# Optimization experiments

Measured on AMD Instinct MI355X. Metric: run time of the kernel, lower is better.

The kernel has to match this reference:

```python
import jax, jax.numpy as jnp
import numpy as np

B, C, H, W = 32, 512, 28, 28
NC, NM, K = 50, 4, 5          # num_classes, num_mixtures, num_clutter_models
OCC = 0.3                     # occ_likely[0]


def setup_inputs() -> dict:
    key = jax.random.key(0)
    k1, k2, k3 = jax.random.split(key, 3)
    x = jax.random.uniform(k1, (B, C, H, W), dtype=jnp.float32)
    mix_model = jax.random.uniform(k2, (NC * NM, C, H, W), dtype=jnp.float32)
    clutter_model = jax.random.uniform(k3, (K, C), dtype=jnp.float32)
    return {"x": x, "mix_model": mix_model, "clutter_model": clutter_model}


def _l1_normalize(a, axis):
    # torch: F.normalize(torch.clamp(a, 0, 1), p=1, dim=axis) with eps=1e-12
    a = jnp.clip(a, 0.0, 1.0)
    return a / jnp.maximum(jnp.sum(a, axis=axis, keepdims=True), 1e-12)


def reference(x, mix_model, clutter_model):
    # clutter: [K, C] -> L1-normalized over channels
    cl = _l1_normalize(clutter_model, axis=1)
    # background log-likelihood: (x.unsqueeze(1) * cl[:, :, None, None]).sum(2)
    bg = jnp.einsum('bchw,kc->bkhw', x, cl)            # [B, K, H, W]
    bg = jnp.log(bg * OCC + 1e-10)
    # mixture models: [M, C, H, W] -> L1-normalized over channels
    mm = _l1_normalize(mix_model, axis=1)
    # foreground log-likelihood: (x.unsqueeze(1) * mm).sum(2)
    fg = jnp.einsum('bchw,mchw->bmhw', x, mm)          # [B, M, H, W]
    fg = jnp.log(fg * (1.0 - OCC) + 1e-10)
    fg = fg.reshape(B, NC, NM, 1, H, W)
    # per-pixel occlusion max between foreground and background, sum over H, W
    per_model = jnp.maximum(fg, bg[:, None, None, :, :, :]).sum((-1, -2))  # [B, NC, NM, K]
    # max over clutter models, then over mixtures
    return per_model.max(axis=-1).max(axis=-1)          # [B, NC]
```

## Files before the change

kernel.cpp:

```cpp
#include <hip/hip_runtime.h>
#include <math.h>

#define Bc  32
#define Cc  512
#define HWc 784
#define Mc  200
#define Kc  5
#define NCc 50

#define PTm   16
#define MTm   16
#define NMB   13
#define NPB   49
#define CKm   32
#define NCHm  16
#define RSTR  18
#define XPL   (32*RSTR)
#define MPL   (16*RSTR)
#define MMBASE (16*XPL)
#define LDSDW (16*XPL + 16*MPL)

typedef short s8v __attribute__((ext_vector_type(8)));
typedef float f4v __attribute__((ext_vector_type(4)));

union F8 { uint2 u2[2]; s8v h; };

__device__ __forceinline__ unsigned f2b(float f) {
    union { float f; unsigned u; } v; v.f = f;
    return (v.u + 0x7FFFu + ((v.u >> 16) & 1u)) >> 16;
}
__device__ __forceinline__ unsigned pk(float lo, float hi) {
    return f2b(lo) | (f2b(hi) << 16);
}

__global__ __launch_bounds__(256) void k_bg(const float* __restrict__ x,
                                            const float* __restrict__ clut,
                                            float* __restrict__ bgpart) {
    __shared__ float cl[Kc * Cc];
    __shared__ float csum[Kc];
    const int t = threadIdx.x;
    for (int i = t; i < Kc * Cc; i += 256) cl[i] = clut[i];
    __syncthreads();
    if (t < 160) {
        const int k = t >> 5, l = t & 31;
        float s = 0.0f;
        for (int c = l; c < Cc; c += 32) s += cl[k * Cc + c];
#pragma unroll
        for (int off = 16; off > 0; off >>= 1) s += __shfl_down(s, off, 32);
        if (l == 0) csum[k] = fmaxf(s, 1e-12f);
    }
    __syncthreads();

    const int b = blockIdx.x;
    const int z = blockIdx.z;
    const int hw = blockIdx.y * 256 + t;
    if (hw < HWc) {
        float acc[Kc] = {0.f, 0.f, 0.f, 0.f, 0.f};
        const int cbase = z * 128;
        const float* xb = x + ((size_t)b * Cc + cbase) * HWc + hw;
#pragma unroll 4
        for (int c = 0; c < 128; ++c) {
            const float xv = xb[c * HWc];
#pragma unroll
            for (int k = 0; k < Kc; ++k) acc[k] = fmaf(xv, cl[k * Cc + cbase + c], acc[k]);
        }
#pragma unroll
        for (int k = 0; k < Kc; ++k)
            bgpart[(((z * Bc + b) * Kc) + k) * HWc + hw] = acc[k] / csum[k];
    }
}

__global__ void k_bgsum(const float* __restrict__ bgpart, float* __restrict__ bgl) {
    const int i = blockIdx.x * 256 + threadIdx.x;
    const int N = Bc * Kc * HWc;
    if (i < N) {
        const float s = bgpart[i] + bgpart[i + N] + bgpart[i + 2 * N] + bgpart[i + 3 * N];
        bgl[i] = logf(0.3f * s + 1e-10f);
    }
}

__global__ __launch_bounds__(256) __attribute__((amdgpu_waves_per_eu(2, 2)))
void k_fg(const float* __restrict__ x, const float* __restrict__ mm,
          float* __restrict__ fg) {
    __shared__ unsigned lds[LDSDW];

    const int t = threadIdx.x;

    const int nwg = NMB * NPB;
    const int q = nwg >> 3, r = nwg & 7;
    const int xcd = blockIdx.x & 7, sidx = blockIdx.x >> 3;
    const int wgid = (xcd < r ? xcd * (q + 1) : r * (q + 1) + (xcd - r) * q) + sidx;
    const int mblk = wgid % NMB;
    const int pix0 = (wgid / NMB) * PTm;

    int xoff[4], xl[4];
#pragma unroll
    for (int g = 0; g < 4; ++g) {
        const int G = t + 256 * g;
        const int qq = G & 3, b = (G >> 2) & 31, cg = G >> 7;
        xoff[g] = (b * Cc + cg * 4) * HWc + pix0 + 4 * qq;
        xl[g]   = 4 * qq * XPL + b * RSTR + cg * 2;
    }
    int moff[2], ml[2];
    float mzero[2];
#pragma unroll
    for (int g = 0; g < 2; ++g) {
        const int G = t + 256 * g;
        const int qq = G & 3, mr = (G >> 2) & 15, cg = (G >> 6) & 7;
        const int mrow = mblk * MTm + mr;
        mzero[g] = (mrow < Mc) ? 1.0f : 0.0f;
        const int mc = (mrow < Mc) ? mrow : (Mc - 1);
        moff[g] = (mc * Cc + cg * 4) * HWc + pix0 + 4 * qq;
        ml[g]   = MMBASE + 4 * qq * MPL + mr * RSTR + cg * 2;
    }

    const int lane = t & 63;
    const int w    = t >> 6;
    const int row18q = (lane & 15) * RSTR + (lane >> 4) * 4;

    f4v accD[4][2], accS[4];
#pragma unroll
    for (int p = 0; p < 4; ++p) {
        accS[p] = (f4v)0.0f;
#pragma unroll
        for (int bt = 0; bt < 2; ++bt) accD[p][bt] = (f4v)0.0f;
    }
    const s8v ones = {0x3F80, 0x3F80, 0x3F80, 0x3F80, 0x3F80, 0x3F80, 0x3F80, 0x3F80};

    float4 LX[4][4], LM[2][4];
#pragma unroll
    for (int g = 0; g < 4; ++g)
#pragma unroll
        for (int cc = 0; cc < 4; ++cc)
            LX[g][cc] = *(const float4*)(x + xoff[g] + cc * HWc);
#pragma unroll
    for (int g = 0; g < 2; ++g)
#pragma unroll
        for (int cc = 0; cc < 4; ++cc)
            LM[g][cc] = *(const float4*)(mm + moff[g] + cc * HWc);
#pragma unroll
    for (int g = 0; g < 4; ++g) xoff[g] += CKm * HWc;
#pragma unroll
    for (int g = 0; g < 2; ++g) moff[g] += CKm * HWc;

#pragma unroll 1
    for (int ch = 0; ch < NCHm; ++ch) {
        __syncthreads();

#pragma unroll
        for (int g = 0; g < 4; ++g) {
            const float* f0 = (const float*)&LX[g][0];
            const float* f1 = (const float*)&LX[g][1];
            const float* f2 = (const float*)&LX[g][2];
            const float* f3 = (const float*)&LX[g][3];
#pragma unroll
            for (int p = 0; p < 4; ++p)
                *(uint2*)&lds[xl[g] + p * XPL] =
                    make_uint2(pk(f0[p], f1[p]), pk(f2[p], f3[p]));
        }
#pragma unroll
        for (int g = 0; g < 2; ++g) {
            const float z = mzero[g];
            const float* f0 = (const float*)&LM[g][0];
            const float* f1 = (const float*)&LM[g][1];
            const float* f2 = (const float*)&LM[g][2];
            const float* f3 = (const float*)&LM[g][3];
#pragma unroll
            for (int p = 0; p < 4; ++p)
                *(uint2*)&lds[ml[g] + p * MPL] =
                    make_uint2(pk(f0[p] * z, f1[p] * z), pk(f2[p] * z, f3[p] * z));
        }

        if (ch + 1 < NCHm) {
#pragma unroll
            for (int g = 0; g < 4; ++g)
#pragma unroll
                for (int cc = 0; cc < 4; ++cc)
                    LX[g][cc] = *(const float4*)(x + xoff[g] + cc * HWc);
#pragma unroll
            for (int g = 0; g < 2; ++g)
#pragma unroll
                for (int cc = 0; cc < 4; ++cc)
                    LM[g][cc] = *(const float4*)(mm + moff[g] + cc * HWc);
#pragma unroll
            for (int g = 0; g < 4; ++g) xoff[g] += CKm * HWc;
#pragma unroll
            for (int g = 0; g < 2; ++g) moff[g] += CKm * HWc;
        }

        __syncthreads();

#pragma unroll
        for (int p = 0; p < 4; ++p) {
            const int pixg = w * 4 + p;
            const unsigned* Xp = &lds[pixg * XPL + row18q];
            const unsigned* Mp = &lds[MMBASE + pixg * MPL + row18q];
            F8 a0, a1, bf;
            a0.u2[0] = *(const uint2*)(Xp);
            a0.u2[1] = *(const uint2*)(Xp + 2);
            a1.u2[0] = *(const uint2*)(Xp + 16 * RSTR);
            a1.u2[1] = *(const uint2*)(Xp + 16 * RSTR + 2);
            bf.u2[0] = *(const uint2*)(Mp);
            bf.u2[1] = *(const uint2*)(Mp + 2);
            accD[p][0] = __builtin_amdgcn_mfma_f32_16x16x32_bf16(a0.h, bf.h, accD[p][0], 0, 0, 0);
            accD[p][1] = __builtin_amdgcn_mfma_f32_16x16x32_bf16(a1.h, bf.h, accD[p][1], 0, 0, 0);
            accS[p]    = __builtin_amdgcn_mfma_f32_16x16x32_bf16(ones, bf.h, accS[p],    0, 0, 0);
        }
    }

    const int m = mblk * MTm + (lane & 15);
    if (m < Mc) {
        const int quad = lane >> 4;
#pragma unroll
        for (int p = 0; p < 4; ++p) {
            const int hw = pix0 + w * 4 + p;
            const float scale = 0.7f / fmaxf(accS[p][0], 1e-12f);
#pragma unroll
            for (int bt = 0; bt < 2; ++bt)
#pragma unroll
                for (int r = 0; r < 4; ++r) {
                    const int b = bt * 16 + quad * 4 + r;
                    fg[((size_t)m * Bc + b) * HWc + hw] =
                        logf(accD[p][bt][r] * scale + 1e-10f);
                }
        }
    }
}

__global__ __launch_bounds__(256) void k_red(const float* __restrict__ fg,
                                             const float* __restrict__ bgl,
                                             float* __restrict__ pm) {
    const int bm = blockIdx.x;
    const int b = bm / Mc;
    const int m = bm % Mc;
    const int t = threadIdx.x;
    const float* fgp = fg + ((size_t)m * Bc + b) * HWc;
    const float* bgb = bgl + (size_t)b * Kc * HWc;

    float s[Kc] = {0.f, 0.f, 0.f, 0.f, 0.f};
    for (int hw = t; hw < HWc; hw += 256) {
        const float f = fgp[hw];
#pragma unroll
        for (int k = 0; k < Kc; ++k) s[k] += fmaxf(f, bgb[k * HWc + hw]);
    }
#pragma unroll
    for (int off = 32; off > 0; off >>= 1) {
#pragma unroll
        for (int k = 0; k < Kc; ++k) s[k] += __shfl_down(s[k], off, 64);
    }
    __shared__ float red[4][Kc];
    const int wv = t >> 6, ln = t & 63;
    if (ln == 0) {
#pragma unroll
        for (int k = 0; k < Kc; ++k) red[wv][k] = s[k];
    }
    __syncthreads();
    if (t == 0) {
        float best = -INFINITY;
#pragma unroll
        for (int k = 0; k < Kc; ++k)
            best = fmaxf(best, red[0][k] + red[1][k] + red[2][k] + red[3][k]);
        pm[bm] = best;
    }
}

__global__ void k_out(const float* __restrict__ pm, float* __restrict__ out) {
    const int i = blockIdx.x * 256 + threadIdx.x;
    if (i < Bc * NCc) {
        const int b = i / NCc, nc = i % NCc;
        const float* p = pm + (size_t)b * Mc + nc * 4;
        out[i] = fmaxf(fmaxf(p[0], p[1]), fmaxf(p[2], p[3]));
    }
}

extern "C" void kernel_launch(void* const* d_in, const int* in_sizes, int n_in,
                              void* d_out, int out_size, void* d_ws, size_t ws_size,
                              hipStream_t stream) {
    const float* x    = (const float*)d_in[0];
    const float* mixm = (const float*)d_in[1];
    const float* clut = (const float*)d_in[2];
    float* out = (float*)d_out;

    float* fg     = (float*)d_ws;
    float* bgpart = fg + (size_t)Mc * Bc * HWc;
    float* bgl    = bgpart + (size_t)4 * Bc * Kc * HWc;
    float* pm     = bgl + (size_t)Bc * Kc * HWc;

    k_bg   <<<dim3(Bc, 4, 4), 256, 0, stream>>>(x, clut, bgpart);
    k_bgsum<<<dim3((Bc * Kc * HWc + 255) / 256), 256, 0, stream>>>(bgpart, bgl);
    k_fg   <<<dim3(NMB * NPB), 256, 0, stream>>>(x, mixm, fg);
    k_red  <<<dim3(Bc * Mc), 256, 0, stream>>>(fg, bgl, pm);
    k_out  <<<dim3(7), 256, 0, stream>>>(pm, out);
}
```

Measured before the change: 560.6 us.

## Fuse background max-sum reduction into MFMA kernel and swizzle LDS layout

The foreground kernel no longer writes the full [M,B,HW] log-likelihood tensor. It computes the log, takes the max against the background log-likelihoods and sums per pixel in registers, then reduces across waves through LDS into per-pixel-block partials. A small second kernel sums those partials and takes the max over clutter models. This removes a large global write and reread of the foreground tensor. The change also replaces row padding with an XOR swizzle in LDS, staggers the x loads into two halves to lower register pressure, and sets launch bounds to 3 blocks, at the cost of a heavier epilogue and extra scattered reads of the background values.

Result: slower. 636.5 us (+13.6%).

```diff
diff --git a/kernel.cpp b/kernel.cpp
--- a/kernel.cpp
+++ b/kernel.cpp
@@ -14,11 +14,12 @@
 #define NPB   49
 #define CKm   32
 #define NCHm  16
-#define RSTR  18
-#define XPL   (32*RSTR)
-#define MPL   (16*RSTR)
+#define XPL   (32*16)
+#define MPL   (16*16)
 #define MMBASE (16*XPL)
 #define LDSDW (16*XPL + 16*MPL)
+
+#define RSH(row) ((((row) >> 1) & 7) << 1)
 
 typedef short s8v __attribute__((ext_vector_type(8)));
 typedef float f4v __attribute__((ext_vector_type(4)));
@@ -79,9 +80,9 @@
     }
 }
 
-__global__ __launch_bounds__(256) __attribute__((amdgpu_waves_per_eu(2, 2)))
+__global__ __launch_bounds__(256, 3)
 void k_fg(const float* __restrict__ x, const float* __restrict__ mm,
-          float* __restrict__ fg) {
+          const float* __restrict__ bgl, float* __restrict__ pm_part) {
     __shared__ unsigned lds[LDSDW];
 
     const int t = threadIdx.x;
@@ -91,7 +92,8 @@
     const int xcd = blockIdx.x & 7, sidx = blockIdx.x >> 3;
     const int wgid = (xcd < r ? xcd * (q + 1) : r * (q + 1) + (xcd - r) * q) + sidx;
     const int mblk = wgid % NMB;
-    const int pix0 = (wgid / NMB) * PTm;
+    const int pb   = wgid / NMB;
+    const int pix0 = pb * PTm;
 
     int xoff[4], xl[4];
 #pragma unroll
@@ -99,7 +101,7 @@
         const int G = t + 256 * g;
         const int qq = G & 3, b = (G >> 2) & 31, cg = G >> 7;
         xoff[g] = (b * Cc + cg * 4) * HWc + pix0 + 4 * qq;
-        xl[g]   = 4 * qq * XPL + b * RSTR + cg * 2;
+        xl[g]   = 4 * qq * XPL + b * 16 + ((cg * 2) ^ RSH(b));
     }
     int moff[2], ml[2];
     float mzero[2];
@@ -111,12 +113,17 @@
         mzero[g] = (mrow < Mc) ? 1.0f : 0.0f;
         const int mc = (mrow < Mc) ? mrow : (Mc - 1);
         moff[g] = (mc * Cc + cg * 4) * HWc + pix0 + 4 * qq;
-        ml[g]   = MMBASE + 4 * qq * MPL + mr * RSTR + cg * 2;
+        ml[g]   = MMBASE + 4 * qq * MPL + mr * 16 + ((cg * 2) ^ RSH(mr));
     }
 
     const int lane = t & 63;
     const int w    = t >> 6;
-    const int row18q = (lane & 15) * RSTR + (lane >> 4) * 4;
+    const int fr   = lane & 15;
+    const int q4   = (lane >> 4) * 4;
+    const int fsw  = RSH(fr);
+    const int d0   = q4 ^ fsw;
+    const int d1   = (q4 + 2) ^ fsw;
+    const int rowbase = fr * 16;
 
     f4v accD[4][2], accS[4];
 #pragma unroll
@@ -127,37 +134,34 @@
     }
     const s8v ones = {0x3F80, 0x3F80, 0x3F80, 0x3F80, 0x3F80, 0x3F80, 0x3F80, 0x3F80};
 
-    float4 LX[4][4], LM[2][4];
-#pragma unroll
-    for (int g = 0; g < 4; ++g)
+    float4 LXa[2][4], LXb[2][4], LM[2][4];
+#pragma unroll
+    for (int g = 0; g < 2; ++g) {
 #pragma unroll
         for (int cc = 0; cc < 4; ++cc)
-            LX[g][cc] = *(const float4*)(x + xoff[g] + cc * HWc);
-#pragma unroll
-    for (int g = 0; g < 2; ++g)
+            LXa[g][cc] = *(const float4*)(x + xoff[g] + cc * HWc);
+        xoff[g] += CKm * HWc;
+    }
+#pragma unroll
+    for (int g = 0; g < 2; ++g) {
 #pragma unroll
         for (int cc = 0; cc < 4; ++cc)
             LM[g][cc] = *(const float4*)(mm + moff[g] + cc * HWc);
-#pragma unroll
-    for (int g = 0; g < 4; ++g) xoff[g] += CKm * HWc;
-#pragma unroll
-    for (int g = 0; g < 2; ++g) moff[g] += CKm * HWc;
+        moff[g] += CKm * HWc;
+    }
 
 #pragma unroll 1
     for (int ch = 0; ch < NCHm; ++ch) {
         __syncthreads();
 
 #pragma unroll
-        for (int g = 0; g < 4; ++g) {
-            const float* f0 = (const float*)&LX[g][0];
-            const float* f1 = (const float*)&LX[g][1];
-            const float* f2 = (const float*)&LX[g][2];
-            const float* f3 = (const float*)&LX[g][3];
-#pragma unroll
-            for (int p = 0; p < 4; ++p)
-                *(uint2*)&lds[xl[g] + p * XPL] =
-                    make_uint2(pk(f0[p], f1[p]), pk(f2[p], f3[p]));
-        }
+        for (int g = 0; g < 2; ++g) {
+#pragma unroll
+            for (int cc = 0; cc < 4; ++cc)
+                LXb[g][cc] = *(const float4*)(x + xoff[g + 2] + cc * HWc);
+            xoff[g + 2] += CKm * HWc;
+        }
+
 #pragma unroll
         for (int g = 0; g < 2; ++g) {
             const float z = mzero[g];
@@ -170,22 +174,47 @@
                 *(uint2*)&lds[ml[g] + p * MPL] =
                     make_uint2(pk(f0[p] * z, f1[p] * z), pk(f2[p] * z, f3[p] * z));
         }
-
         if (ch + 1 < NCHm) {
 #pragma unroll
-            for (int g = 0; g < 4; ++g)
-#pragma unroll
-                for (int cc = 0; cc < 4; ++cc)
-                    LX[g][cc] = *(const float4*)(x + xoff[g] + cc * HWc);
-#pragma unroll
-            for (int g = 0; g < 2; ++g)
+            for (int g = 0; g < 2; ++g) {
 #pragma unroll
                 for (int cc = 0; cc < 4; ++cc)
                     LM[g][cc] = *(const float4*)(mm + moff[g] + cc * HWc);
-#pragma unroll
-            for (int g = 0; g < 4; ++g) xoff[g] += CKm * HWc;
-#pragma unroll
-            for (int g = 0; g < 2; ++g) moff[g] += CKm * HWc;
+                moff[g] += CKm * HWc;
+            }
+        }
+
+#pragma unroll
+        for (int g = 0; g < 2; ++g) {
+            const float* f0 = (const float*)&LXa[g][0];
+            const float* f1 = (const float*)&LXa[g][1];
+            const float* f2 = (const float*)&LXa[g][2];
+            const float* f3 = (const float*)&LXa[g][3];
+#pragma unroll
+            for (int p = 0; p < 4; ++p)
+                *(uint2*)&lds[xl[g] + p * XPL] =
+                    make_uint2(pk(f0[p], f1[p]), pk(f2[p], f3[p]));
+        }
+        if (ch + 1 < NCHm) {
+#pragma unroll
+            for (int g = 0; g < 2; ++g) {
+#pragma unroll
+                for (int cc = 0; cc < 4; ++cc)
+                    LXa[g][cc] = *(const float4*)(x + xoff[g] + cc * HWc);
+                xoff[g] += CKm * HWc;
+            }
+        }
+
+#pragma unroll
+        for (int g = 0; g < 2; ++g) {
+            const float* f0 = (const float*)&LXb[g][0];
+            const float* f1 = (const float*)&LXb[g][1];
+            const float* f2 = (const float*)&LXb[g][2];
+            const float* f3 = (const float*)&LXb[g][3];
+#pragma unroll
+            for (int p = 0; p < 4; ++p)
+                *(uint2*)&lds[xl[g + 2] + p * XPL] =
+                    make_uint2(pk(f0[p], f1[p]), pk(f2[p], f3[p]));
         }
 
         __syncthreads();
@@ -193,74 +222,93 @@
 #pragma unroll
         for (int p = 0; p < 4; ++p) {
             const int pixg = w * 4 + p;
-            const unsigned* Xp = &lds[pixg * XPL + row18q];
-            const unsigned* Mp = &lds[MMBASE + pixg * MPL + row18q];
+            const unsigned* Xp = &lds[pixg * XPL + rowbase];
+            const unsigned* Mp = &lds[MMBASE + pixg * MPL + rowbase];
             F8 a0, a1, bf;
-            a0.u2[0] = *(const uint2*)(Xp);
-            a0.u2[1] = *(const uint2*)(Xp + 2);
-            a1.u2[0] = *(const uint2*)(Xp + 16 * RSTR);
-            a1.u2[1] = *(const uint2*)(Xp + 16 * RSTR + 2);
-            bf.u2[0] = *(const uint2*)(Mp);
-            bf.u2[1] = *(const uint2*)(Mp + 2);
+            a0.u2[0] = *(const uint2*)(Xp + d0);
+            a0.u2[1] = *(const uint2*)(Xp + d1);
+            a1.u2[0] = *(const uint2*)(Xp + 256 + d0);
+            a1.u2[1] = *(const uint2*)(Xp + 256 + d1);
+            bf.u2[0] = *(const uint2*)(Mp + d0);
+            bf.u2[1] = *(const uint2*)(Mp + d1);
             accD[p][0] = __builtin_amdgcn_mfma_f32_16x16x32_bf16(a0.h, bf.h, accD[p][0], 0, 0, 0);
             accD[p][1] = __builtin_amdgcn_mfma_f32_16x16x32_bf16(a1.h, bf.h, accD[p][1], 0, 0, 0);
             accS[p]    = __builtin_amdgcn_mfma_f32_16x16x32_bf16(ones, bf.h, accS[p],    0, 0, 0);
         }
     }
 
-    const int m = mblk * MTm + (lane & 15);
-    if (m < Mc) {
-        const int quad = lane >> 4;
-#pragma unroll
-        for (int p = 0; p < 4; ++p) {
-            const int hw = pix0 + w * 4 + p;
-            const float scale = 0.7f / fmaxf(accS[p][0], 1e-12f);
-#pragma unroll
-            for (int bt = 0; bt < 2; ++bt)
-#pragma unroll
-                for (int r = 0; r < 4; ++r) {
-                    const int b = bt * 16 + quad * 4 + r;
-                    fg[((size_t)m * Bc + b) * HWc + hw] =
-                        logf(accD[p][bt][r] * scale + 1e-10f);
-                }
-        }
-    }
-}
-
-__global__ __launch_bounds__(256) void k_red(const float* __restrict__ fg,
-                                             const float* __restrict__ bgl,
-                                             float* __restrict__ pm) {
-    const int bm = blockIdx.x;
-    const int b = bm / Mc;
-    const int m = bm % Mc;
-    const int t = threadIdx.x;
-    const float* fgp = fg + ((size_t)m * Bc + b) * HWc;
-    const float* bgb = bgl + (size_t)b * Kc * HWc;
-
-    float s[Kc] = {0.f, 0.f, 0.f, 0.f, 0.f};
-    for (int hw = t; hw < HWc; hw += 256) {
-        const float f = fgp[hw];
-#pragma unroll
-        for (int k = 0; k < Kc; ++k) s[k] += fmaxf(f, bgb[k * HWc + hw]);
-    }
-#pragma unroll
-    for (int off = 32; off > 0; off >>= 1) {
-#pragma unroll
-        for (int k = 0; k < Kc; ++k) s[k] += __shfl_down(s[k], off, 64);
-    }
-    __shared__ float red[4][Kc];
-    const int wv = t >> 6, ln = t & 63;
-    if (ln == 0) {
-#pragma unroll
-        for (int k = 0; k < Kc; ++k) red[wv][k] = s[k];
-    }
+    const int quad = lane >> 4;
+    float S[2][4][Kc];
+#pragma unroll
+    for (int bt = 0; bt < 2; ++bt)
+#pragma unroll
+        for (int rr = 0; rr < 4; ++rr)
+#pragma unroll
+            for (int k = 0; k < Kc; ++k) S[bt][rr][k] = 0.0f;
+
+#pragma unroll
+    for (int p = 0; p < 4; ++p) {
+        const int hw = pix0 + w * 4 + p;
+        const float scale = 0.7f / fmaxf(accS[p][0], 1e-12f);
+#pragma unroll
+        for (int bt = 0; bt < 2; ++bt)
+#pragma unroll
+            for (int rr = 0; rr < 4; ++rr) {
+                const float fgv = logf(accD[p][bt][rr] * scale + 1e-10f);
+                const int b = bt * 16 + quad * 4 + rr;
+                const float* bp = bgl + (size_t)b * Kc * HWc + hw;
+#pragma unroll
+                for (int k = 0; k < Kc; ++k)
+                    S[bt][rr][k] += fmaxf(fgv, bp[k * HWc]);
+            }
+    }
+
     __syncthreads();
-    if (t == 0) {
-        float best = -INFINITY;
-#pragma unroll
-        for (int k = 0; k < Kc; ++k)
-            best = fmaxf(best, red[0][k] + red[1][k] + red[2][k] + red[3][k]);
-        pm[bm] = best;
+    float* ldsf = (float*)lds;
+    {
+        float* dst = ldsf + (w * 64 + lane) * 40;
+#pragma unroll
+        for (int bt = 0; bt < 2; ++bt)
+#pragma unroll
+            for (int rr = 0; rr < 4; ++rr)
+#pragma unroll
+                for (int k = 0; k < Kc; ++k)
+                    dst[(bt * 4 + rr) * Kc + k] = S[bt][rr][k];
+    }
+    __syncthreads();
+
+#pragma unroll
+    for (int j = 0; j < 10; ++j) {
+        const int o = t * 10 + j;
+        const int k = o % Kc;
+        const int b = (o / Kc) & 31;
+        const int mloc = o / (Kc * 32);
+        const int m = mblk * MTm + mloc;
+        if (m < Mc) {
+            const int lsel = ((b >> 2) & 3) * 16 + mloc;
+            const int ji = ((b >> 4) * 4 + (b & 3)) * Kc + k;
+            float v = ldsf[(0 * 64 + lsel) * 40 + ji]
+                    + ldsf[(1 * 64 + lsel) * 40 + ji]
+                    + ldsf[(2 * 64 + lsel) * 40 + ji]
+                    + ldsf[(3 * 64 + lsel) * 40 + ji];
+            pm_part[(((size_t)pb * Bc + b) * Kc + k) * Mc + m] = v;
+        }
+    }
+}
+
+__global__ __launch_bounds__(256) void k_red2(const float* __restrict__ pm_part,
+                                              float* __restrict__ pm) {
+    const int i = blockIdx.x * 256 + threadIdx.x;
+    if (i < Bc * Mc) {
+        const int b = i / Mc, m = i % Mc;
+        float s[Kc] = {0.f, 0.f, 0.f, 0.f, 0.f};
+        for (int pb = 0; pb < NPB; ++pb) {
+            const float* p = pm_part + (((size_t)pb * Bc + b) * Kc) * Mc + m;
+#pragma unroll
+            for (int k = 0; k < Kc; ++k) s[k] += p[k * Mc];
+        }
+        const float best = fmaxf(fmaxf(fmaxf(s[0], s[1]), fmaxf(s[2], s[3])), s[4]);
+        pm[(size_t)b * Mc + m] = best;
     }
 }
 
@@ -281,14 +329,14 @@
     const float* clut = (const float*)d_in[2];
     float* out = (float*)d_out;
 
-    float* fg     = (float*)d_ws;
-    float* bgpart = fg + (size_t)Mc * Bc * HWc;
+    float* bgpart = (float*)d_ws;
     float* bgl    = bgpart + (size_t)4 * Bc * Kc * HWc;
-    float* pm     = bgl + (size_t)Bc * Kc * HWc;
+    float* pmpart = bgl + (size_t)Bc * Kc * HWc;
+    float* pm     = pmpart + (size_t)NPB * Bc * Kc * Mc;
 
     k_bg   <<<dim3(Bc, 4, 4), 256, 0, stream>>>(x, clut, bgpart);
     k_bgsum<<<dim3((Bc * Kc * HWc + 255) / 256), 256, 0, stream>>>(bgpart, bgl);
-    k_fg   <<<dim3(NMB * NPB), 256, 0, stream>>>(x, mixm, fg);
-    k_red  <<<dim3(Bc * Mc), 256, 0, stream>>>(fg, bgl, pm);
+    k_fg   <<<dim3(NMB * NPB), 256, 0, stream>>>(x, mixm, bgl, pmpart);
+    k_red2 <<<dim3((Bc * Mc + 255) / 256), 256, 0, stream>>>(pmpart, pm);
     k_out  <<<dim3(7), 256, 0, stream>>>(pm, out);
 }
```
